# Kernel optimization log

Hardware: AMD Instinct MI355X
Metric: run time of the kernel (lower is better)

## Reference

```python
import jax, jax.numpy as jnp
import numpy as np

B = 65536          # batch rows
FULL = 1024        # full_dim
E = 64             # number of block experts
W = FULL // E      # block width = 16 (equal contiguous slices)
HID = 64           # expert hidden
GH = 32            # gate hidden
SCALE = 0.05


def setup_inputs() -> dict:
    key = jax.random.key(0)
    ks = jax.random.split(key, 12)
    n = jax.random.normal
    return {
        "x": n(ks[0], (B, FULL), dtype=jnp.float32),
        # gate: Linear(FULL,32) -> ReLU -> Linear(32,E)
        "gw1": n(ks[1], (FULL, GH), dtype=jnp.float32) * SCALE,
        "gb1": n(ks[2], (GH,), dtype=jnp.float32) * SCALE,
        "gw2": n(ks[3], (GH, E), dtype=jnp.float32) * SCALE,
        "gb2": n(ks[4], (E,), dtype=jnp.float32) * SCALE,
        # stacked per-expert MLP params: W->HID->HID//2->1
        "ew1": n(ks[5], (E, W, HID), dtype=jnp.float32) * SCALE,
        "eb1": n(ks[6], (E, HID), dtype=jnp.float32) * SCALE,
        "ew2": n(ks[7], (E, HID, HID // 2), dtype=jnp.float32) * SCALE,
        "eb2": n(ks[8], (E, HID // 2), dtype=jnp.float32) * SCALE,
        "ew3": n(ks[9], (E, HID // 2, 1), dtype=jnp.float32) * SCALE,
        "eb3": n(ks[10], (E, 1), dtype=jnp.float32) * SCALE,
    }


def reference(x, gw1, gb1, gw2, gb2, ew1, eb1, ew2, eb2, ew3, eb3):
    # gate -> soft weights over experts, [B, E]
    g = jax.nn.relu(x @ gw1 + gb1)
    w = jax.nn.softmax(g @ gw2 + gb2, axis=1)
    # equal contiguous blocks: x[:, e*W:(e+1)*W] == x.reshape(B, E, W)[:, e]
    xb = x.reshape(x.shape[0], E, W)
    h = jax.nn.relu(jnp.einsum("bew,ewh->beh", xb, ew1) + eb1)      # [B,E,HID]
    h = jax.nn.relu(jnp.einsum("beh,eho->beo", h, ew2) + eb2)       # [B,E,HID//2]
    logits = (jnp.einsum("beh,eho->beo", h, ew3) + eb3)[..., 0]     # [B,E]
    return jnp.sum(w * logits, axis=1, keepdims=True)               # [B,1]
```

## Files before the change

### kernel.cpp

```cpp
#include <hip/hip_runtime.h>

typedef __attribute__((ext_vector_type(8))) short short8;
typedef __attribute__((ext_vector_type(4))) short short4_;
typedef __attribute__((ext_vector_type(4))) float float4_;

#define NGROUP 16
#define EPG 4
#define GBLK_US 14336
#define OFF_A2_US 4096
#define OFF_AG_US 12288
#define OFF_TAIL_US 229376
#define N_A1 65536
#define N_A2 131072
#define N_AG 32768
#define N_TOT 231424

__device__ __forceinline__ unsigned short f2bf(float f) {
  unsigned u = __builtin_bit_cast(unsigned, f);
  u += 0x7FFFu + ((u >> 16) & 1u);
  return (unsigned short)(u >> 16);
}
__device__ __forceinline__ float bf2f(unsigned short s) {
  unsigned u = ((unsigned)s) << 16;
  return __builtin_bit_cast(float, u);
}
__device__ __forceinline__ float4_ MFMA(short8 a, short8 b, float4_ c) {
  return __builtin_amdgcn_mfma_f32_16x16x32_bf16(a, b, c, 0, 0, 0);
}
__device__ __forceinline__ float4_ relu4(float4_ v) {
  v[0] = fmaxf(v[0], 0.f); v[1] = fmaxf(v[1], 0.f);
  v[2] = fmaxf(v[2], 0.f); v[3] = fmaxf(v[3], 0.f);
  return v;
}
__device__ __forceinline__ short8 swap32(short8 v) {
  union { short8 s; int i[4]; } u; u.s = v;
#pragma unroll
  for (int k = 0; k < 4; ++k) u.i[k] = __shfl_xor(u.i[k], 32);
  return u.s;
}

__global__ void moe_setup(const float* __restrict__ gw1,
                          const float* __restrict__ gw2,
                          const float* __restrict__ ew1,
                          const float* __restrict__ ew2,
                          unsigned short* __restrict__ wsp)
{
  for (int i = blockIdx.x * blockDim.x + threadIdx.x; i < N_TOT;
       i += gridDim.x * blockDim.x) {
    if (i < N_A1) {
      int g = i >> 12, a = i & 4095;
      int j = a & 7, l = (a >> 3) & 31, mt = (a >> 8) & 3, e = (a >> 10) & 3;
      int k = ((l >> 4) << 3) + j;
      int h = 16 * mt + (l & 15);
      int E = g * 4 + e;
      wsp[g * GBLK_US + a] = f2bf(ew1[(E * 16 + k) * 64 + h]);
    } else if (i < N_A1 + N_A2) {
      int i2 = i - N_A1;
      int g = i2 >> 13, b = i2 & 8191;
      int j = b & 3, l = (b >> 2) & 63, c = (b >> 8) & 3, mt2 = (b >> 10) & 1, e = (b >> 11) & 3;
      int q = l >> 4;
      int h1 = 16 * c + 4 * q + j;
      int h2 = 16 * mt2 + (l & 15);
      int E = g * 4 + e;
      wsp[g * GBLK_US + OFF_A2_US + b] = f2bf(ew2[(E * 64 + h1) * 32 + h2]);
    } else if (i < N_A1 + N_A2 + N_AG) {
      int i3 = i - (N_A1 + N_A2);
      int g = i3 >> 11, a = i3 & 2047;
      int j = a & 7, l = (a >> 3) & 63, kc = (a >> 9) & 1, mt = (a >> 10) & 1;
      int q = l >> 4;
      int col = g * 64 + kc * 32 + q * 8 + j;
      int gh = 16 * mt + (l & 15);
      wsp[g * GBLK_US + OFF_AG_US + a] = f2bf(gw1[col * 32 + gh]);
    } else {
      int d = i - (N_A1 + N_A2 + N_AG);
      int j = d & 3, l = (d >> 2) & 63, c = (d >> 8) & 1, mt3 = (d >> 9) & 3;
      int q = l >> 4;
      int gh = 16 * c + 4 * q + j;
      int e = 16 * mt3 + (l & 15);
      wsp[OFF_TAIL_US + d] = f2bf(gw2[gh * 64 + e]);
    }
  }
}

__global__ __launch_bounds__(512, 2) void moe_main(
    const float* __restrict__ x,
    const float* __restrict__ gb1,
    const float* __restrict__ gb2,
    const float* __restrict__ eb1,
    const float* __restrict__ eb2,
    const float* __restrict__ ew3,
    const float* __restrict__ eb3,
    const unsigned short* __restrict__ wsp,
    float* __restrict__ out)
{
  __shared__ __align__(16) unsigned short sStage[GBLK_US];
  __shared__ unsigned short sStash[64 * 256];

  const int tid = threadIdx.x;
  const int wave = tid >> 6;
  const int lane = tid & 63;
  const int q = lane >> 4;
  const int n = lane & 15;
  const int wrow = wave * 32;
  const size_t rowBase0 = (size_t)blockIdx.x * 256 + wrow;

  const short8 zero8 = {0, 0, 0, 0, 0, 0, 0, 0};

  float4_ cg[2][2];
#pragma unroll
  for (int t = 0; t < 2; ++t)
#pragma unroll
    for (int m = 0; m < 2; ++m) cg[t][m] = (float4_){0.f, 0.f, 0.f, 0.f};

  for (int g = 0; g < NGROUP; ++g) {
    __syncthreads();
    {
      const uint4* src = (const uint4*)(wsp + (size_t)g * GBLK_US);
      uint4* dst = (uint4*)sStage;
#pragma unroll
      for (int it = 0; it < 4; ++it) {
        int idx = tid + it * 512;
        if (idx < 1792) dst[idx] = src[idx];
      }
    }
    __syncthreads();

    short8 bx[2][2];
#pragma unroll
    for (int t = 0; t < 2; ++t)
#pragma unroll
      for (int kc = 0; kc < 2; ++kc) {
        const float* px = x + (rowBase0 + t * 16 + n) * 1024 + g * 64 + kc * 32 + q * 8;
        float4_ f0 = *(const float4_*)px;
        float4_ f1 = *(const float4_*)(px + 4);
        short8 v;
        v[0] = f2bf(f0[0]); v[1] = f2bf(f0[1]); v[2] = f2bf(f0[2]); v[3] = f2bf(f0[3]);
        v[4] = f2bf(f1[0]); v[5] = f2bf(f1[1]); v[6] = f2bf(f1[2]); v[7] = f2bf(f1[3]);
        bx[t][kc] = v;
      }

#pragma unroll
    for (int m = 0; m < 2; ++m)
#pragma unroll
      for (int kc = 0; kc < 2; ++kc) {
        short8 a = *(const short8*)(sStage + OFF_AG_US + ((m * 2 + kc) * 64 + lane) * 8);
        cg[0][m] = MFMA(a, bx[0][kc], cg[0][m]);
        cg[1][m] = MFMA(a, bx[1][kc], cg[1][m]);
      }

    for (int e = 0; e < EPG; ++e) {
      const int E = g * EPG + e;
      short8 b1[2];
#pragma unroll
      for (int t = 0; t < 2; ++t) {
        short8 src = bx[t][e >> 1];
        if (e & 1) src = swap32(src);
        b1[t] = (lane < 32) ? src : zero8;
      }
      float4_ c1[2][4];
#pragma unroll
      for (int m = 0; m < 4; ++m) {
        float4_ bi = *(const float4_*)(eb1 + E * 64 + 16 * m + 4 * q);
        c1[0][m] = bi; c1[1][m] = bi;
      }
#pragma unroll
      for (int m = 0; m < 4; ++m) {
        short8 a1 = zero8;
        if (lane < 32) a1 = *(const short8*)(sStage + ((e * 4 + m) * 32 + lane) * 8);
        c1[0][m] = MFMA(a1, b1[0], c1[0][m]);
        c1[1][m] = MFMA(a1, b1[1], c1[1][m]);
      }
#pragma unroll
      for (int t = 0; t < 2; ++t)
#pragma unroll
        for (int m = 0; m < 4; ++m) c1[t][m] = relu4(c1[t][m]);

      float4_ c2[2][2];
#pragma unroll
      for (int m = 0; m < 2; ++m) {
        float4_ bi = *(const float4_*)(eb2 + E * 32 + 16 * m + 4 * q);
        c2[0][m] = bi; c2[1][m] = bi;
      }
#pragma unroll
      for (int c = 0; c < 4; ++c) {
        short8 b2[2];
#pragma unroll
        for (int t = 0; t < 2; ++t) {
          short8 v = zero8;
          v[0] = f2bf(c1[t][c][0]); v[1] = f2bf(c1[t][c][1]);
          v[2] = f2bf(c1[t][c][2]); v[3] = f2bf(c1[t][c][3]);
          b2[t] = v;
        }
#pragma unroll
        for (int m = 0; m < 2; ++m) {
          short4_ lo = *(const short4_*)(sStage + OFF_A2_US + (((e * 2 + m) * 4 + c) * 64 + lane) * 4);
          short8 a2 = {lo[0], lo[1], lo[2], lo[3], 0, 0, 0, 0};
          c2[0][m] = MFMA(a2, b2[0], c2[0][m]);
          c2[1][m] = MFMA(a2, b2[1], c2[1][m]);
        }
      }
#pragma unroll
      for (int t = 0; t < 2; ++t) {
        float p = 0.f;
#pragma unroll
        for (int m = 0; m < 2; ++m) {
          float4_ cc = relu4(c2[t][m]);
          float4_ w3v = *(const float4_*)(ew3 + E * 32 + 16 * m + 4 * q);
          p += cc[0] * w3v[0] + cc[1] * w3v[1] + cc[2] * w3v[2] + cc[3] * w3v[3];
        }
        p += __shfl_xor(p, 16);
        p += __shfl_xor(p, 32);
        p += eb3[E];
        if (lane < 16) sStash[E * 256 + wrow + t * 16 + lane] = f2bf(p);
      }
    }
  }

#pragma unroll
  for (int t = 0; t < 2; ++t) {
    short8 bg[2];
#pragma unroll
    for (int c = 0; c < 2; ++c) {
      float4_ gv = *(const float4_*)(gb1 + 16 * c + 4 * q);
      float4_ v = cg[t][c];
      v[0] = fmaxf(v[0] + gv[0], 0.f); v[1] = fmaxf(v[1] + gv[1], 0.f);
      v[2] = fmaxf(v[2] + gv[2], 0.f); v[3] = fmaxf(v[3] + gv[3], 0.f);
      short8 pv = zero8;
      pv[0] = f2bf(v[0]); pv[1] = f2bf(v[1]); pv[2] = f2bf(v[2]); pv[3] = f2bf(v[3]);
      bg[c] = pv;
    }
    float4_ c3[4];
#pragma unroll
    for (int m = 0; m < 4; ++m)
      c3[m] = *(const float4_*)(gb2 + 16 * m + 4 * q);
#pragma unroll
    for (int m = 0; m < 4; ++m)
#pragma unroll
      for (int c = 0; c < 2; ++c) {
        short4_ lo = *(const short4_*)(wsp + OFF_TAIL_US + ((m * 2 + c) * 64 + lane) * 4);
        short8 a = {lo[0], lo[1], lo[2], lo[3], 0, 0, 0, 0};
        c3[m] = MFMA(a, bg[c], c3[m]);
      }
    float mx = -1e30f;
#pragma unroll
    for (int m = 0; m < 4; ++m) {
      mx = fmaxf(mx, c3[m][0]); mx = fmaxf(mx, c3[m][1]);
      mx = fmaxf(mx, c3[m][2]); mx = fmaxf(mx, c3[m][3]);
    }
    mx = fmaxf(mx, __shfl_xor(mx, 16));
    mx = fmaxf(mx, __shfl_xor(mx, 32));
    float s = 0.f, o = 0.f;
#pragma unroll
    for (int m = 0; m < 4; ++m)
#pragma unroll
      for (int i = 0; i < 4; ++i) {
        int e = 16 * m + 4 * q + i;
        float w = __expf(c3[m][i] - mx);
        s += w;
        o += w * bf2f(sStash[e * 256 + wrow + t * 16 + n]);
      }
    s += __shfl_xor(s, 16);
    s += __shfl_xor(s, 32);
    o += __shfl_xor(o, 16);
    o += __shfl_xor(o, 32);
    if (lane < 16) out[rowBase0 + t * 16 + lane] = o / s;
  }
}

extern "C" void kernel_launch(void* const* d_in, const int* in_sizes, int n_in,
                              void* d_out, int out_size, void* d_ws, size_t ws_size,
                              hipStream_t stream) {
  const float* x   = (const float*)d_in[0];
  const float* gw1 = (const float*)d_in[1];
  const float* gb1 = (const float*)d_in[2];
  const float* gw2 = (const float*)d_in[3];
  const float* gb2 = (const float*)d_in[4];
  const float* ew1 = (const float*)d_in[5];
  const float* eb1 = (const float*)d_in[6];
  const float* ew2 = (const float*)d_in[7];
  const float* eb2 = (const float*)d_in[8];
  const float* ew3 = (const float*)d_in[9];
  const float* eb3 = (const float*)d_in[10];
  unsigned short* wsp = (unsigned short*)d_ws;
  float* out = (float*)d_out;

  moe_setup<<<256, 256, 0, stream>>>(gw1, gw2, ew1, ew2, wsp);
  moe_main<<<256, 512, 0, stream>>>(x, gb1, gb2, eb1, eb2, ew3, eb3, wsp, out);
}
```

Before: 502.3 us.

## Halve rows per wave and block to double grid and raise occupancy

Each wave now processes 16 rows instead of 32, and each block covers 128 rows, so the grid doubles to 512 blocks. Launch bounds are raised to 4 blocks per CU and the stash buffer shrinks with a padded stride of 130. The aim is to fill the whole GPU (256 blocks left many CUs underused) and add latency hiding through more resident waves. In exchange, each staged weight group is reused by half as many rows, so weight staging traffic and sync overhead per row double, and register pressure is bounded more tightly.

```diff
diff --git a/kernel.cpp b/kernel.cpp
--- a/kernel.cpp
+++ b/kernel.cpp
@@ -14,6 +14,9 @@
 #define N_A2 131072
 #define N_AG 32768
 #define N_TOT 231424
+
+#define ROWS_PB 128
+#define STASH_LD 130
 
 __device__ __forceinline__ unsigned short f2bf(float f) {
   unsigned u = __builtin_bit_cast(unsigned, f);
@@ -82,7 +85,7 @@
   }
 }
 
-__global__ __launch_bounds__(512, 2) void moe_main(
+__global__ __launch_bounds__(512, 4) void moe_main(
     const float* __restrict__ x,
     const float* __restrict__ gb1,
     const float* __restrict__ gb2,
@@ -94,23 +97,21 @@
     float* __restrict__ out)
 {
   __shared__ __align__(16) unsigned short sStage[GBLK_US];
-  __shared__ unsigned short sStash[64 * 256];
+  __shared__ unsigned short sStash[64 * STASH_LD];
 
   const int tid = threadIdx.x;
   const int wave = tid >> 6;
   const int lane = tid & 63;
   const int q = lane >> 4;
   const int n = lane & 15;
-  const int wrow = wave * 32;
-  const size_t rowBase0 = (size_t)blockIdx.x * 256 + wrow;
+  const int wrow = wave * 16;
+  const size_t rowBase0 = (size_t)blockIdx.x * ROWS_PB + wrow;
 
   const short8 zero8 = {0, 0, 0, 0, 0, 0, 0, 0};
 
-  float4_ cg[2][2];
-#pragma unroll
-  for (int t = 0; t < 2; ++t)
-#pragma unroll
-    for (int m = 0; m < 2; ++m) cg[t][m] = (float4_){0.f, 0.f, 0.f, 0.f};
+  float4_ cg[2];
+  cg[0] = (float4_){0.f, 0.f, 0.f, 0.f};
+  cg[1] = (float4_){0.f, 0.f, 0.f, 0.f};
 
   for (int g = 0; g < NGROUP; ++g) {
     __syncthreads();
@@ -125,146 +126,121 @@
     }
     __syncthreads();
 
-    short8 bx[2][2];
-#pragma unroll
-    for (int t = 0; t < 2; ++t)
-#pragma unroll
-      for (int kc = 0; kc < 2; ++kc) {
-        const float* px = x + (rowBase0 + t * 16 + n) * 1024 + g * 64 + kc * 32 + q * 8;
-        float4_ f0 = *(const float4_*)px;
-        float4_ f1 = *(const float4_*)(px + 4);
-        short8 v;
-        v[0] = f2bf(f0[0]); v[1] = f2bf(f0[1]); v[2] = f2bf(f0[2]); v[3] = f2bf(f0[3]);
-        v[4] = f2bf(f1[0]); v[5] = f2bf(f1[1]); v[6] = f2bf(f1[2]); v[7] = f2bf(f1[3]);
-        bx[t][kc] = v;
-      }
+    short8 bx[2];
+#pragma unroll
+    for (int kc = 0; kc < 2; ++kc) {
+      const float* px = x + (rowBase0 + n) * 1024 + g * 64 + kc * 32 + q * 8;
+      float4_ f0 = *(const float4_*)px;
+      float4_ f1 = *(const float4_*)(px + 4);
+      short8 v;
+      v[0] = f2bf(f0[0]); v[1] = f2bf(f0[1]); v[2] = f2bf(f0[2]); v[3] = f2bf(f0[3]);
+      v[4] = f2bf(f1[0]); v[5] = f2bf(f1[1]); v[6] = f2bf(f1[2]); v[7] = f2bf(f1[3]);
+      bx[kc] = v;
+    }
 
 #pragma unroll
     for (int m = 0; m < 2; ++m)
 #pragma unroll
       for (int kc = 0; kc < 2; ++kc) {
         short8 a = *(const short8*)(sStage + OFF_AG_US + ((m * 2 + kc) * 64 + lane) * 8);
-        cg[0][m] = MFMA(a, bx[0][kc], cg[0][m]);
-        cg[1][m] = MFMA(a, bx[1][kc], cg[1][m]);
+        cg[m] = MFMA(a, bx[kc], cg[m]);
       }
 
     for (int e = 0; e < EPG; ++e) {
       const int E = g * EPG + e;
-      short8 b1[2];
-#pragma unroll
-      for (int t = 0; t < 2; ++t) {
-        short8 src = bx[t][e >> 1];
-        if (e & 1) src = swap32(src);
-        b1[t] = (lane < 32) ? src : zero8;
-      }
-      float4_ c1[2][4];
-#pragma unroll
-      for (int m = 0; m < 4; ++m) {
-        float4_ bi = *(const float4_*)(eb1 + E * 64 + 16 * m + 4 * q);
-        c1[0][m] = bi; c1[1][m] = bi;
-      }
+      short8 b1 = bx[e >> 1];
+      if (e & 1) b1 = swap32(b1);
+      b1 = (lane < 32) ? b1 : zero8;
+
+      float4_ c1[4];
+#pragma unroll
+      for (int m = 0; m < 4; ++m)
+        c1[m] = *(const float4_*)(eb1 + E * 64 + 16 * m + 4 * q);
 #pragma unroll
       for (int m = 0; m < 4; ++m) {
         short8 a1 = zero8;
         if (lane < 32) a1 = *(const short8*)(sStage + ((e * 4 + m) * 32 + lane) * 8);
-        c1[0][m] = MFMA(a1, b1[0], c1[0][m]);
-        c1[1][m] = MFMA(a1, b1[1], c1[1][m]);
-      }
-#pragma unroll
-      for (int t = 0; t < 2; ++t)
-#pragma unroll
-        for (int m = 0; m < 4; ++m) c1[t][m] = relu4(c1[t][m]);
-
-      float4_ c2[2][2];
-#pragma unroll
-      for (int m = 0; m < 2; ++m) {
-        float4_ bi = *(const float4_*)(eb2 + E * 32 + 16 * m + 4 * q);
-        c2[0][m] = bi; c2[1][m] = bi;
-      }
+        c1[m] = MFMA(a1, b1, c1[m]);
+      }
+#pragma unroll
+      for (int m = 0; m < 4; ++m) c1[m] = relu4(c1[m]);
+
+      float4_ c2[2];
+#pragma unroll
+      for (int m = 0; m < 2; ++m)
+        c2[m] = *(const float4_*)(eb2 + E * 32 + 16 * m + 4 * q);
 #pragma unroll
       for (int c = 0; c < 4; ++c) {
-        short8 b2[2];
-#pragma unroll
-        for (int t = 0; t < 2; ++t) {
-          short8 v = zero8;
-          v[0] = f2bf(c1[t][c][0]); v[1] = f2bf(c1[t][c][1]);
-          v[2] = f2bf(c1[t][c][2]); v[3] = f2bf(c1[t][c][3]);
-          b2[t] = v;
-        }
+        short8 b2 = zero8;
+        b2[0] = f2bf(c1[c][0]); b2[1] = f2bf(c1[c][1]);
+        b2[2] = f2bf(c1[c][2]); b2[3] = f2bf(c1[c][3]);
 #pragma unroll
         for (int m = 0; m < 2; ++m) {
           short4_ lo = *(const short4_*)(sStage + OFF_A2_US + (((e * 2 + m) * 4 + c) * 64 + lane) * 4);
           short8 a2 = {lo[0], lo[1], lo[2], lo[3], 0, 0, 0, 0};
-          c2[0][m] = MFMA(a2, b2[0], c2[0][m]);
-          c2[1][m] = MFMA(a2, b2[1], c2[1][m]);
+          c2[m] = MFMA(a2, b2, c2[m]);
         }
       }
-#pragma unroll
-      for (int t = 0; t < 2; ++t) {
-        float p = 0.f;
-#pragma unroll
-        for (int m = 0; m < 2; ++m) {
-          float4_ cc = relu4(c2[t][m]);
-          float4_ w3v = *(const float4_*)(ew3 + E * 32 + 16 * m + 4 * q);
-          p += cc[0] * w3v[0] + cc[1] * w3v[1] + cc[2] * w3v[2] + cc[3] * w3v[3];
-        }
-        p += __shfl_xor(p, 16);
-        p += __shfl_xor(p, 32);
-        p += eb3[E];
-        if (lane < 16) sStash[E * 256 + wrow + t * 16 + lane] = f2bf(p);
-      }
-    }
-  }
-
-#pragma unroll
-  for (int t = 0; t < 2; ++t) {
-    short8 bg[2];
+      float p = 0.f;
+#pragma unroll
+      for (int m = 0; m < 2; ++m) {
+        float4_ cc = relu4(c2[m]);
+        float4_ w3v = *(const float4_*)(ew3 + E * 32 + 16 * m + 4 * q);
+        p += cc[0] * w3v[0] + cc[1] * w3v[1] + cc[2] * w3v[2] + cc[3] * w3v[3];
+      }
+      p += __shfl_xor(p, 16);
+      p += __shfl_xor(p, 32);
+      p += eb3[E];
+      if (lane < 16) sStash[E * STASH_LD + wrow + lane] = f2bf(p);
+    }
+  }
+
+  short8 bg[2];
+#pragma unroll
+  for (int c = 0; c < 2; ++c) {
+    float4_ gv = *(const float4_*)(gb1 + 16 * c + 4 * q);
+    float4_ v = cg[c];
+    v[0] = fmaxf(v[0] + gv[0], 0.f); v[1] = fmaxf(v[1] + gv[1], 0.f);
+    v[2] = fmaxf(v[2] + gv[2], 0.f); v[3] = fmaxf(v[3] + gv[3], 0.f);
+    short8 pv = zero8;
+    pv[0] = f2bf(v[0]); pv[1] = f2bf(v[1]); pv[2] = f2bf(v[2]); pv[3] = f2bf(v[3]);
+    bg[c] = pv;
+  }
+  float4_ c3[4];
+#pragma unroll
+  for (int m = 0; m < 4; ++m)
+    c3[m] = *(const float4_*)(gb2 + 16 * m + 4 * q);
+#pragma unroll
+  for (int m = 0; m < 4; ++m)
 #pragma unroll
     for (int c = 0; c < 2; ++c) {
-      float4_ gv = *(const float4_*)(gb1 + 16 * c + 4 * q);
-      float4_ v = cg[t][c];
-      v[0] = fmaxf(v[0] + gv[0], 0.f); v[1] = fmaxf(v[1] + gv[1], 0.f);
-      v[2] = fmaxf(v[2] + gv[2], 0.f); v[3] = fmaxf(v[3] + gv[3], 0.f);
-      short8 pv = zero8;
-      pv[0] = f2bf(v[0]); pv[1] = f2bf(v[1]); pv[2] = f2bf(v[2]); pv[3] = f2bf(v[3]);
-      bg[c] = pv;
-    }
-    float4_ c3[4];
-#pragma unroll
-    for (int m = 0; m < 4; ++m)
-      c3[m] = *(const float4_*)(gb2 + 16 * m + 4 * q);
-#pragma unroll
-    for (int m = 0; m < 4; ++m)
-#pragma unroll
-      for (int c = 0; c < 2; ++c) {
-        short4_ lo = *(const short4_*)(wsp + OFF_TAIL_US + ((m * 2 + c) * 64 + lane) * 4);
-        short8 a = {lo[0], lo[1], lo[2], lo[3], 0, 0, 0, 0};
-        c3[m] = MFMA(a, bg[c], c3[m]);
-      }
-    float mx = -1e30f;
-#pragma unroll
-    for (int m = 0; m < 4; ++m) {
-      mx = fmaxf(mx, c3[m][0]); mx = fmaxf(mx, c3[m][1]);
-      mx = fmaxf(mx, c3[m][2]); mx = fmaxf(mx, c3[m][3]);
-    }
-    mx = fmaxf(mx, __shfl_xor(mx, 16));
-    mx = fmaxf(mx, __shfl_xor(mx, 32));
-    float s = 0.f, o = 0.f;
-#pragma unroll
-    for (int m = 0; m < 4; ++m)
-#pragma unroll
-      for (int i = 0; i < 4; ++i) {
-        int e = 16 * m + 4 * q + i;
-        float w = __expf(c3[m][i] - mx);
-        s += w;
-        o += w * bf2f(sStash[e * 256 + wrow + t * 16 + n]);
-      }
-    s += __shfl_xor(s, 16);
-    s += __shfl_xor(s, 32);
-    o += __shfl_xor(o, 16);
-    o += __shfl_xor(o, 32);
-    if (lane < 16) out[rowBase0 + t * 16 + lane] = o / s;
-  }
+      short4_ lo = *(const short4_*)(wsp + OFF_TAIL_US + ((m * 2 + c) * 64 + lane) * 4);
+      short8 a = {lo[0], lo[1], lo[2], lo[3], 0, 0, 0, 0};
+      c3[m] = MFMA(a, bg[c], c3[m]);
+    }
+  float mx = -1e30f;
+#pragma unroll
+  for (int m = 0; m < 4; ++m) {
+    mx = fmaxf(mx, c3[m][0]); mx = fmaxf(mx, c3[m][1]);
+    mx = fmaxf(mx, c3[m][2]); mx = fmaxf(mx, c3[m][3]);
+  }
+  mx = fmaxf(mx, __shfl_xor(mx, 16));
+  mx = fmaxf(mx, __shfl_xor(mx, 32));
+  float s = 0.f, o = 0.f;
+#pragma unroll
+  for (int m = 0; m < 4; ++m)
+#pragma unroll
+    for (int i = 0; i < 4; ++i) {
+      int e = 16 * m + 4 * q + i;
+      float w = __expf(c3[m][i] - mx);
+      s += w;
+      o += w * bf2f(sStash[e * STASH_LD + wrow + n]);
+    }
+  s += __shfl_xor(s, 16);
+  s += __shfl_xor(s, 32);
+  o += __shfl_xor(o, 16);
+  o += __shfl_xor(o, 32);
+  if (lane < 16) out[rowBase0 + lane] = o / s;
 }
 
 extern "C" void kernel_launch(void* const* d_in, const int* in_sizes, int n_in,
@@ -285,5 +261,5 @@
   float* out = (float*)d_out;
 
   moe_setup<<<256, 256, 0, stream>>>(gw1, gw2, ew1, ew2, wsp);
-  moe_main<<<256, 512, 0, stream>>>(x, gb1, gb2, eb1, eb2, ew3, eb3, wsp, out);
-}
+  moe_main<<<512, 512, 0, stream>>>(x, gb1, gb2, eb1, eb2, ew3, eb3, wsp, out);
+}
```

Result: faster. 462.2 us (-8.0%).
